# Kernel optimization log

Measured on AMD Instinct MI355X. Metric: run time of the kernel, lower is better.

The kernel has to match this reference:

```python
import jax, jax.numpy as jnp
import numpy as np

N = 100000   # nodes
E = 3200000  # edges
M = 4096     # moves
K = 16       # orders per move
NEG_SLOPE = 0.2  # PyG GATv2Conv default negative_slope

PARAM_SHAPES = {
    'g1_Wl': (10, 15), 'g1_Wr': (10, 15), 'g1_att': (10,), 'g1_b': (10,),
    'g2_Wl': (10, 25), 'g2_Wr': (10, 25), 'g2_att': (10,), 'g2_b': (10,),
    'g3_Wl': (10, 25), 'g3_Wr': (10, 25), 'g3_att': (10,), 'g3_b': (10,),
    'vt_W': (20, 29), 'vt_b': (20,), 'va_W': (1, 20), 'va_b': (1,),
    'vv_W': (10, 20), 'vv_b': (10,), 'vl_W': (1, 10), 'vl_b': (1,),
    'at_W': (20, 48), 'at_b': (20,), 'dt_W': (20, 23), 'dt_b': (20,),
    'oa_W': (1, 20), 'oa_b': (1,), 'ov_W': (1, 20), 'ov_b': (1,),
}
PARAM_NAMES = list(PARAM_SHAPES.keys())


def _linear(x, W, b):
    return x @ W.T + b


def _gatv2(x, src, dst, Wl, Wr, att, b):
    # GATv2Conv (heads=1, self-loops appended by caller), eval mode (no dropout)
    xl = x @ Wl.T  # messages from source nodes
    xr = x @ Wr.T
    e = (jax.nn.leaky_relu(xl[src] + xr[dst], NEG_SLOPE) * att).sum(-1)  # [E+N]
    emax = jax.ops.segment_max(e, dst, num_segments=N)
    ee = jnp.exp(e - emax[dst])
    denom = jax.ops.segment_sum(ee, dst, num_segments=N)
    alpha = ee / denom[dst]
    return jax.ops.segment_sum(alpha[:, None] * xl[src], dst, num_segments=N) + b


def _forward(x1, x2, edges, move_src, move_dst, move_armies, is_attack, params):
    (g1_Wl, g1_Wr, g1_att, g1_b,
     g2_Wl, g2_Wr, g2_att, g2_b,
     g3_Wl, g3_Wr, g3_att, g3_b,
     vt_W, vt_b, va_W, va_b, vv_W, vv_b, vl_W, vl_b,
     at_W, at_b, dt_W, dt_b, oa_W, oa_b, ov_W, ov_b) = params
    x2t = jnp.tile(x2, (N, 1))  # [N,4]
    self_idx = jnp.arange(N, dtype=edges.dtype)
    src = jnp.concatenate([edges[0], self_idx])
    dst = jnp.concatenate([edges[1], self_idx])
    x = jax.nn.relu(_gatv2(x1, src, dst, g1_Wl, g1_Wr, g1_att, g1_b))
    x = jax.nn.relu(_gatv2(jnp.concatenate([x, x1], 1), src, dst, g2_Wl, g2_Wr, g2_att, g2_b))
    x = jax.nn.relu(_gatv2(jnp.concatenate([x, x1], 1), src, dst, g3_Wl, g3_Wr, g3_att, g3_b))  # [N,10]
    # per-move order tensors (vectorized over [M,K]); deploy uses move_src as target
    xs, xd = x[move_src], x[move_dst]       # [M,K,10]
    x1s, x1d = x1[move_src], x1[move_dst]   # [M,K,15]
    extra = 0.6 * move_armies - 0.7 * (x1d[..., 3] + x1d[..., 4])
    attack_in = jnp.concatenate([xs, xd, x1s[..., 3:], x1d[..., 1:],
                                 move_armies[..., None], extra[..., None]], -1)  # [M,K,48]
    deploy_in = jnp.concatenate([xs, x1s[..., 3:], move_armies[..., None]], -1)  # [M,K,23]
    feat = jnp.where(is_attack[..., None] == 1,
                     _linear(attack_in, at_W, at_b),
                     _linear(deploy_in, dt_W, dt_b))
    feat = jax.nn.relu(feat)  # dropout = identity (eval)
    attn = jax.nn.softmax(_linear(feat, oa_W, oa_b), axis=1)  # softmax over orders
    p = (attn * _linear(feat, ov_W, ov_b)).sum(axis=(1, 2))   # [M]
    # value head: attention pooling over all nodes
    Vn = jax.nn.relu(_linear(jnp.concatenate([x, x1, x2t], 1), vt_W, vt_b))  # [N,20]
    vatt = jax.nn.softmax(_linear(Vn, va_W, va_b), axis=0)
    Vp = jax.nn.relu((vatt * _linear(Vn, vv_W, vv_b)).sum(axis=0))
    V = jnp.tanh(_linear(Vp, vl_W, vl_b))[0]
    return V, jax.nn.log_softmax(p, axis=0)


def setup_inputs() -> dict:
    key = jax.random.key(0)
    ks = iter(jax.random.split(key, 64))
    inp = {
        'x1': jax.random.normal(next(ks), (N, 15), jnp.float32),
        'x2': jax.random.normal(next(ks), (4,), jnp.float32),
        'edges': jax.random.randint(next(ks), (2, E), 0, N, jnp.int32),
        'move_src': jax.random.randint(next(ks), (M, K), 0, N, jnp.int32),
        'move_dst': jax.random.randint(next(ks), (M, K), 0, N, jnp.int32),
        'move_armies': jax.random.uniform(next(ks), (M, K), jnp.float32) * 10.0,
        'is_attack': jax.random.randint(next(ks), (M, K), 0, 2, jnp.int32),
    }
    for name, shape in PARAM_SHAPES.items():
        inp[name] = jax.random.normal(next(ks), shape, jnp.float32) * 0.1
    return inp


def reference(x1, x2, edges, move_src, move_dst, move_armies, is_attack,
              g1_Wl, g1_Wr, g1_att, g1_b, g2_Wl, g2_Wr, g2_att, g2_b,
              g3_Wl, g3_Wr, g3_att, g3_b, vt_W, vt_b, va_W, va_b,
              vv_W, vv_b, vl_W, vl_b, at_W, at_b, dt_W, dt_b,
              oa_W, oa_b, ov_W, ov_b):
    params = (g1_Wl, g1_Wr, g1_att, g1_b, g2_Wl, g2_Wr, g2_att, g2_b,
              g3_Wl, g3_Wr, g3_att, g3_b, vt_W, vt_b, va_W, va_b,
              vv_W, vv_b, vl_W, vl_b, at_W, at_b, dt_W, dt_b,
              oa_W, oa_b, ov_W, ov_b)
    return _forward(x1, x2, edges, move_src, move_dst, move_armies, is_attack, params)
```

## Files before the change

### kernel.cpp

```cpp
#include <hip/hip_runtime.h>
#include <hip/hip_fp16.h>
#include <math.h>

#define NN 100000
#define NE 3200000
#define MM 4096
#define KK 16
#define NEG_SLOPE 0.2f
#define SUB 8
#define BSH 8
#define NB 391
#define PCH 4096
#define FCAP 9728
#define XS 12
#define XSU 4
#define PART_BLOCKS ((NE + NN + PCH - 1) / PCH)
#define LIN_BLOCKS  ((NN + 255) / 256)
#define MOVE_BLOCKS ((MM * KK) / 256)
#define VAL_BLOCKS  ((NN + 255) / 256)
#define CSTR 16
#define PZ ((int)0xAAAAAAAAu)

typedef float vfloat2 __attribute__((__vector_size__(2 * sizeof(float))));

__device__ __forceinline__ void f8x10_decode(const uint4& w, float* xs) {
    vfloat2 f0 = __builtin_amdgcn_cvt_pk_f32_fp8(w.x, false); xs[0]=f0[0]; xs[1]=f0[1];
    vfloat2 f1 = __builtin_amdgcn_cvt_pk_f32_fp8(w.x, true);  xs[2]=f1[0]; xs[3]=f1[1];
    vfloat2 f2 = __builtin_amdgcn_cvt_pk_f32_fp8(w.y, false); xs[4]=f2[0]; xs[5]=f2[1];
    vfloat2 f3 = __builtin_amdgcn_cvt_pk_f32_fp8(w.y, true);  xs[6]=f3[0]; xs[7]=f3[1];
    vfloat2 f4 = __builtin_amdgcn_cvt_pk_f32_fp8(w.z, false); xs[8]=f4[0]; xs[9]=f4[1];
}
__device__ __forceinline__ uint4 f8x10_encode(const float* v) {
    unsigned u0 = __builtin_amdgcn_cvt_pk_fp8_f32(v[0], v[1], 0, false);
    u0 = __builtin_amdgcn_cvt_pk_fp8_f32(v[2], v[3], u0, true);
    unsigned u1 = __builtin_amdgcn_cvt_pk_fp8_f32(v[4], v[5], 0, false);
    u1 = __builtin_amdgcn_cvt_pk_fp8_f32(v[6], v[7], u1, true);
    unsigned u2 = __builtin_amdgcn_cvt_pk_fp8_f32(v[8], v[9], 0, false);
    return make_uint4(u0, u1, u2, 0u);
}

__global__ __launch_bounds__(256) void part_lin1_kernel(const int* __restrict__ edges,
                                                        int* __restrict__ cnt,
                                                        unsigned* __restrict__ recs,
                                                        const float* __restrict__ x1,
                                                        const float* __restrict__ Wl,
                                                        const float* __restrict__ Wr,
                                                        unsigned* __restrict__ xl8,
                                                        float* __restrict__ xr) {
    int t = threadIdx.x;
    if (blockIdx.x >= PART_BLOCKS) {
        int i = (blockIdx.x - PART_BLOCKS) * 256 + t;
        if (i >= NN) return;
        float in[15];
        #pragma unroll
        for (int j = 0; j < 15; j++) in[j] = x1[(long)i * 15 + j];
        float sl[10];
        #pragma unroll
        for (int o = 0; o < 10; o++) {
            float l = 0.f, r = 0.f;
            #pragma unroll
            for (int j = 0; j < 15; j++) {
                l += Wl[o * 15 + j] * in[j];
                r += Wr[o * 15 + j] * in[j];
            }
            sl[o] = l;
            xr[(long)i * XS + o] = r;
        }
        *(uint4*)(xl8 + (long)i * XSU) = f8x10_encode(sl);
        return;
    }
    __shared__ unsigned srt[PCH];
    __shared__ unsigned short sbk[PCH];
    __shared__ int scn[512];
    __shared__ int h[NB];
    __shared__ int gb[NB];
    __shared__ int cur[NB];
    __shared__ int lb[NB];
    const int total = NE + NN;
    int base = blockIdx.x * PCH;
    int n = min(PCH, total - base);
    for (int b = t; b < NB; b += 256) { h[b] = 0; cur[b] = 0; }
    __syncthreads();
    for (int j = t; j < n; j += 256) {
        int i = base + j;
        int d = (i < NE) ? edges[NE + i] : (i - NE);
        atomicAdd(&h[d >> BSH], 1);
    }
    __syncthreads();
    for (int b = t; b < NB; b += 256) {
        int hv = h[b];
        if (hv > 0) gb[b] = atomicAdd(&cnt[b * CSTR], hv) - PZ;
    }
    scn[t]       = (t < NB)       ? h[t]       : 0;
    scn[t + 256] = (t + 256 < NB) ? h[t + 256] : 0;
    __syncthreads();
    for (int off = 1; off < 512; off <<= 1) {
        int v0 = (t >= off)       ? scn[t - off]       : 0;
        int v1 = (t + 256 >= off) ? scn[t + 256 - off] : 0;
        __syncthreads();
        scn[t] += v0; scn[t + 256] += v1;
        __syncthreads();
    }
    if (t < NB)       lb[t]       = scn[t]       - h[t];
    if (t + 256 < NB) lb[t + 256] = scn[t + 256] - h[t + 256];
    __syncthreads();
    for (int j = t; j < n; j += 256) {
        int i = base + j;
        int s, d;
        if (i < NE) { s = edges[i]; d = edges[NE + i]; }
        else        { s = i - NE; d = s; }
        int b = d >> BSH;
        int slot = lb[b] + atomicAdd(&cur[b], 1);
        srt[slot] = ((unsigned)(d & 255) << 17) | (unsigned)s;
        sbk[slot] = (unsigned short)b;
    }
    __syncthreads();
    for (int j = t; j < n; j += 256) {
        int b = sbk[j];
        int gpos = gb[b] + (j - lb[b]);
        if (gpos >= 0 && gpos < FCAP) recs[(long)b * FCAP + gpos] = srt[j];
    }
}

__global__ __launch_bounds__(1024) void fine_sort_kernel(const unsigned* __restrict__ recs,
                                                         const int* __restrict__ cnt,
                                                         int* __restrict__ csr_src,
                                                         int* __restrict__ offsets) {
    __shared__ unsigned srt2[FCAP];
    __shared__ int scn[512];
    __shared__ int hist[256];
    __shared__ int sc[256];
    __shared__ int hb[257];
    __shared__ int cur[256];
    int b = blockIdx.x;
    int t = threadIdx.x;
    int c = 0;
    if (t < 512) {
        c = (t < NB) ? min(max(cnt[t * CSTR] - PZ, 0), FCAP) : 0;
        scn[t] = c;
    }
    __syncthreads();
    for (int off = 1; off < 512; off <<= 1) {
        int v = 0;
        if (t < 512 && t >= off) v = scn[t - off];
        __syncthreads();
        if (t < 512) scn[t] += v;
        __syncthreads();
    }
    int beg = (b == 0) ? 0 : scn[b - 1];
    int nb = min(max(cnt[b * CSTR] - PZ, 0), FCAP);
    int nodebase = b << BSH;
    int nnodes = min(256, NN - nodebase);
    if (t < 256) { hist[t] = 0; cur[t] = 0; }
    __syncthreads();
    const unsigned* rsrc = recs + (long)b * FCAP;
    for (int j = t; j < nb; j += 1024)
        atomicAdd(&hist[rsrc[j] >> 17], 1);
    __syncthreads();
    int hv = (t < 256) ? hist[t] : 0;
    if (t < 256) sc[t] = hv;
    __syncthreads();
    for (int off = 1; off < 256; off <<= 1) {
        int v = 0;
        if (t < 256 && t >= off) v = sc[t - off];
        __syncthreads();
        if (t < 256) sc[t] += v;
        __syncthreads();
    }
    if (t < 256) hb[t] = sc[t] - hv;
    if (t == 0) hb[256] = nb;
    __syncthreads();
    for (int j = t; j < nb; j += 1024) {
        unsigned r = rsrc[j];
        int l = r >> 17;
        int p = hb[l] + atomicAdd(&cur[l], 1);
        srt2[p] = r & 0x1FFFFu;
    }
    __syncthreads();
    for (int j = t; j < nb; j += 1024)
        csr_src[beg + j] = (int)srt2[j];
    if (t < nnodes) offsets[nodebase + t] = beg + hb[t];
    if (b == NB - 1 && t == 0) offsets[NN] = beg + nb;
}

template<bool FUSE_NEXT>
__global__ void gat_aggregate_kernel(const int* __restrict__ csr_src,
                                     const int* __restrict__ offsets,
                                     const unsigned* __restrict__ xl8,
                                     const float* __restrict__ xr,
                                     const float* __restrict__ att,
                                     const float* __restrict__ b,
                                     const float* __restrict__ x1,
                                     const float* __restrict__ nWl,
                                     const float* __restrict__ nWr,
                                     unsigned* __restrict__ xlo,
                                     float* __restrict__ xro,
                                     float* __restrict__ xout)
{
    int t = blockIdx.x * blockDim.x + threadIdx.x;
    int node = t / SUB;
    int lane = t % SUB;
    if (node >= NN) return;
    float xrn[12], a[10];
    const float4* xr4 = (const float4*)(xr + (long)node * XS);
    #pragma unroll
    for (int q = 0; q < 3; q++) {
        float4 v = xr4[q];
        xrn[4*q] = v.x; xrn[4*q+1] = v.y; xrn[4*q+2] = v.z; xrn[4*q+3] = v.w;
    }
    #pragma unroll
    for (int h = 0; h < 10; h++) a[h] = att[h];
    int beg = offsets[node], end = offsets[node + 1];
    float den = 0.f, num[10];
    #pragma unroll
    for (int h = 0; h < 10; h++) num[h] = 0.f;
    int j = beg + lane;
    for (; j + 3 * SUB < end; j += 4 * SUB) {
        int s0 = csr_src[j];
        int s1 = csr_src[j + SUB];
        int s2 = csr_src[j + 2 * SUB];
        int s3 = csr_src[j + 3 * SUB];
        uint4 wa[4];
        wa[0] = *(const uint4*)(xl8 + (long)s0 * XSU);
        wa[1] = *(const uint4*)(xl8 + (long)s1 * XSU);
        wa[2] = *(const uint4*)(xl8 + (long)s2 * XSU);
        wa[3] = *(const uint4*)(xl8 + (long)s3 * XSU);
        #pragma unroll
        for (int q = 0; q < 4; q++) {
            float xs[10];
            f8x10_decode(wa[q], xs);
            float e = 0.f;
            #pragma unroll
            for (int h = 0; h < 10; h++) {
                float v = xs[h] + xrn[h];
                v = (v >= 0.f) ? v : NEG_SLOPE * v;
                e += v * a[h];
            }
            float w = __expf(e);
            den += w;
            #pragma unroll
            for (int h = 0; h < 10; h++) num[h] += w * xs[h];
        }
    }
    for (; j < end; j += SUB) {
        int s = csr_src[j];
        uint4 wa = *(const uint4*)(xl8 + (long)s * XSU);
        float xs[10];
        f8x10_decode(wa, xs);
        float e = 0.f;
        #pragma unroll
        for (int h = 0; h < 10; h++) {
            float v = xs[h] + xrn[h];
            v = (v >= 0.f) ? v : NEG_SLOPE * v;
            e += v * a[h];
        }
        float w = __expf(e);
        den += w;
        #pragma unroll
        for (int h = 0; h < 10; h++) num[h] += w * xs[h];
    }
    #pragma unroll
    for (int off = SUB / 2; off; off >>= 1) {
        den += __shfl_xor(den, off, SUB);
        #pragma unroll
        for (int h = 0; h < 10; h++) num[h] += __shfl_xor(num[h], off, SUB);
    }
    float inv = 1.f / den;
    float xo[10];
    #pragma unroll
    for (int h = 0; h < 10; h++) xo[h] = fmaxf(num[h] * inv + b[h], 0.f);
    if (FUSE_NEXT) {
        if (lane < 5) {
            float in2[25];
            #pragma unroll
            for (int h = 0; h < 10; h++) in2[h] = xo[h];
            #pragma unroll
            for (int h = 0; h < 15; h++) in2[10 + h] = x1[(long)node * 15 + h];
            int o0 = 2 * lane, o1 = 2 * lane + 1;
            float sl0 = 0.f, sl1 = 0.f, sr0 = 0.f, sr1 = 0.f;
            #pragma unroll
            for (int jj = 0; jj < 25; jj++) {
                sl0 += nWl[o0 * 25 + jj] * in2[jj];
                sl1 += nWl[o1 * 25 + jj] * in2[jj];
                sr0 += nWr[o0 * 25 + jj] * in2[jj];
                sr1 += nWr[o1 * 25 + jj] * in2[jj];
            }
            unsigned pk = __builtin_amdgcn_cvt_pk_fp8_f32(sl0, sl1, 0, false);
            ((unsigned short*)(xlo + (long)node * XSU))[lane] = (unsigned short)pk;
            *(float2*)(xro + (long)node * XS + o0) = make_float2(sr0, sr1);
        }
    } else {
        if (lane == 0) {
            #pragma unroll
            for (int h = 0; h < 10; h++) xout[(long)node * XS + h] = xo[h];
        }
    }
}

__global__ void move_value_kernel(const float* __restrict__ x,
                                  const float* __restrict__ x1,
                                  const float* __restrict__ x2,
                                  const int* __restrict__ msrc,
                                  const int* __restrict__ mdst,
                                  const float* __restrict__ armies,
                                  const int* __restrict__ isatk,
                                  const float* __restrict__ at_W, const float* __restrict__ at_b,
                                  const float* __restrict__ dt_W, const float* __restrict__ dt_b,
                                  const float* __restrict__ oa_W, const float* __restrict__ oa_b,
                                  const float* __restrict__ ov_W, const float* __restrict__ ov_b,
                                  const float* __restrict__ vt_W, const float* __restrict__ vt_b,
                                  const float* __restrict__ va_W, const float* __restrict__ va_b,
                                  const float* __restrict__ vv_W, const float* __restrict__ vv_b,
                                  float* __restrict__ p,
                                  float* __restrict__ partials) {
    if (blockIdx.x < MOVE_BLOCKS) {
        int t = blockIdx.x * 256 + threadIdx.x;
        int m = t >> 4;
        int k = t & 15;
        int s = msrc[t], d = mdst[t];
        float arm = armies[t];
        bool atk = (isatk[t] == 1);
        float xsrc[12];
        const float4* xs4 = (const float4*)(x + (long)s * XS);
        #pragma unroll
        for (int q = 0; q < 3; q++) {
            float4 v = xs4[q];
            xsrc[4*q]=v.x; xsrc[4*q+1]=v.y; xsrc[4*q+2]=v.z; xsrc[4*q+3]=v.w;
        }
        float feat[20];
        if (atk) {
            float in[48];
            #pragma unroll
            for (int h = 0; h < 10; h++) in[h] = xsrc[h];
            const float4* xd4 = (const float4*)(x + (long)d * XS);
            float xdst[12];
            #pragma unroll
            for (int q = 0; q < 3; q++) {
                float4 v = xd4[q];
                xdst[4*q]=v.x; xdst[4*q+1]=v.y; xdst[4*q+2]=v.z; xdst[4*q+3]=v.w;
            }
            #pragma unroll
            for (int h = 0; h < 10; h++) in[10 + h] = xdst[h];
            #pragma unroll
            for (int h = 0; h < 12; h++) in[20 + h] = x1[(long)s * 15 + 3 + h];
            #pragma unroll
            for (int h = 0; h < 14; h++) in[32 + h] = x1[(long)d * 15 + 1 + h];
            in[46] = arm;
            in[47] = 0.6f * arm - 0.7f * (x1[(long)d * 15 + 3] + x1[(long)d * 15 + 4]);
            #pragma unroll
            for (int o = 0; o < 20; o++) {
                float sum = at_b[o];
                #pragma unroll
                for (int j = 0; j < 48; j++) sum += at_W[o * 48 + j] * in[j];
                feat[o] = fmaxf(sum, 0.f);
            }
        } else {
            float in[23];
            #pragma unroll
            for (int h = 0; h < 10; h++) in[h] = xsrc[h];
            #pragma unroll
            for (int h = 0; h < 12; h++) in[10 + h] = x1[(long)s * 15 + 3 + h];
            in[22] = arm;
            #pragma unroll
            for (int o = 0; o < 20; o++) {
                float sum = dt_b[o];
                #pragma unroll
                for (int j = 0; j < 23; j++) sum += dt_W[o * 23 + j] * in[j];
                feat[o] = fmaxf(sum, 0.f);
            }
        }
        float oa = oa_b[0], ov = ov_b[0];
        #pragma unroll
        for (int j = 0; j < 20; j++) {
            oa += oa_W[j] * feat[j];
            ov += ov_W[j] * feat[j];
        }
        float mx = oa;
        #pragma unroll
        for (int off = 8; off; off >>= 1) mx = fmaxf(mx, __shfl_xor(mx, off, 16));
        float w = __expf(oa - mx);
        float nume = w * ov;
        float den = w;
        #pragma unroll
        for (int off = 8; off; off >>= 1) {
            nume += __shfl_xor(nume, off, 16);
            den  += __shfl_xor(den,  off, 16);
        }
        if (k == 0) p[m] = nume / den;
        return;
    }
    __shared__ float sm[4][11];
    int vb = blockIdx.x - MOVE_BLOCKS;
    int i = vb * 256 + threadIdx.x;
    float w = 0.f;
    float acc[10];
    #pragma unroll
    for (int h = 0; h < 10; h++) acc[h] = 0.f;
    if (i < NN) {
        float in[29];
        const float4* xi4 = (const float4*)(x + (long)i * XS);
        float xi[12];
        #pragma unroll
        for (int q = 0; q < 3; q++) {
            float4 v = xi4[q];
            xi[4*q]=v.x; xi[4*q+1]=v.y; xi[4*q+2]=v.z; xi[4*q+3]=v.w;
        }
        #pragma unroll
        for (int h = 0; h < 10; h++) in[h] = xi[h];
        #pragma unroll
        for (int h = 0; h < 15; h++) in[10 + h] = x1[(long)i * 15 + h];
        #pragma unroll
        for (int h = 0; h < 4; h++) in[25 + h] = x2[h];
        float Vn[20];
        #pragma unroll
        for (int o = 0; o < 20; o++) {
            float s = vt_b[o];
            #pragma unroll
            for (int j = 0; j < 29; j++) s += vt_W[o * 29 + j] * in[j];
            Vn[o] = fmaxf(s, 0.f);
        }
        float lg = va_b[0];
        #pragma unroll
        for (int j = 0; j < 20; j++) lg += va_W[j] * Vn[j];
        w = __expf(lg);
        #pragma unroll
        for (int o = 0; o < 10; o++) {
            float s = vv_b[o];
            #pragma unroll
            for (int j = 0; j < 20; j++) s += vv_W[o * 20 + j] * Vn[j];
            acc[o] = w * s;
        }
    }
    #pragma unroll
    for (int off = 32; off; off >>= 1) {
        w += __shfl_xor(w, off, 64);
        #pragma unroll
        for (int h = 0; h < 10; h++) acc[h] += __shfl_xor(acc[h], off, 64);
    }
    int wid = threadIdx.x >> 6;
    if ((threadIdx.x & 63) == 0) {
        #pragma unroll
        for (int h = 0; h < 10; h++) sm[wid][h] = acc[h];
        sm[wid][10] = w;
    }
    __syncthreads();
    if (threadIdx.x < 11) {
        int c = threadIdx.x;
        partials[(long)vb * 12 + c] = sm[0][c] + sm[1][c] + sm[2][c] + sm[3][c];
    }
}

__global__ void final_kernel(const float* __restrict__ p,
                             const float* __restrict__ partials,
                             const float* __restrict__ vl_W, const float* __restrict__ vl_b,
                             float* __restrict__ out) {
    if (blockIdx.x == 0) {
        __shared__ float sm[256];
        int tid = threadIdx.x;
        float mx = -INFINITY;
        for (int i = tid; i < MM; i += 256) mx = fmaxf(mx, p[i]);
        sm[tid] = mx; __syncthreads();
        for (int s = 128; s; s >>= 1) { if (tid < s) sm[tid] = fmaxf(sm[tid], sm[tid + s]); __syncthreads(); }
        mx = sm[0]; __syncthreads();
        float sum = 0.f;
        for (int i = tid; i < MM; i += 256) sum += expf(p[i] - mx);
        sm[tid] = sum; __syncthreads();
        for (int s = 128; s; s >>= 1) { if (tid < s) sm[tid] += sm[tid + s]; __syncthreads(); }
        float ls = mx + logf(sm[0]);
        for (int i = tid; i < MM; i += 256) out[1 + i] = p[i] - ls;
    } else if (threadIdx.x < 64) {
        int lane = threadIdx.x;
        float s[11];
        #pragma unroll
        for (int c = 0; c < 11; c++) s[c] = 0.f;
        for (int j = lane; j < VAL_BLOCKS; j += 64)
            #pragma unroll
            for (int c = 0; c < 11; c++) s[c] += partials[(long)j * 12 + c];
        #pragma unroll
        for (int off = 32; off; off >>= 1)
            #pragma unroll
            for (int c = 0; c < 11; c++) s[c] += __shfl_xor(s[c], off, 64);
        if (lane == 0) {
            float inv = 1.0f / s[10];
            float v = vl_b[0];
            #pragma unroll
            for (int h = 0; h < 10; h++) v += vl_W[h] * fmaxf(s[h] * inv, 0.f);
            out[0] = tanhf(v);
        }
    }
}

extern "C" void kernel_launch(void* const* d_in, const int* in_sizes, int n_in,
                              void* d_out, int out_size, void* d_ws, size_t ws_size,
                              hipStream_t stream) {
    const float* x1      = (const float*)d_in[0];
    const float* x2      = (const float*)d_in[1];
    const int*   edges   = (const int*)d_in[2];
    const int*   msrc    = (const int*)d_in[3];
    const int*   mdst    = (const int*)d_in[4];
    const float* armies  = (const float*)d_in[5];
    const int*   isatk   = (const int*)d_in[6];
    const float* g1_Wl = (const float*)d_in[7],  *g1_Wr = (const float*)d_in[8];
    const float* g1_att= (const float*)d_in[9],  *g1_b  = (const float*)d_in[10];
    const float* g2_Wl = (const float*)d_in[11], *g2_Wr = (const float*)d_in[12];
    const float* g2_att= (const float*)d_in[13], *g2_b  = (const float*)d_in[14];
    const float* g3_Wl = (const float*)d_in[15], *g3_Wr = (const float*)d_in[16];
    const float* g3_att= (const float*)d_in[17], *g3_b  = (const float*)d_in[18];
    const float* vt_W  = (const float*)d_in[19], *vt_b  = (const float*)d_in[20];
    const float* va_W  = (const float*)d_in[21], *va_b  = (const float*)d_in[22];
    const float* vv_W  = (const float*)d_in[23], *vv_b  = (const float*)d_in[24];
    const float* vl_W  = (const float*)d_in[25], *vl_b  = (const float*)d_in[26];
    const float* at_W  = (const float*)d_in[27], *at_b  = (const float*)d_in[28];
    const float* dt_W  = (const float*)d_in[29], *dt_b  = (const float*)d_in[30];
    const float* oa_W  = (const float*)d_in[31], *oa_b  = (const float*)d_in[32];
    const float* ov_W  = (const float*)d_in[33], *ov_b  = (const float*)d_in[34];

    float* out = (float*)d_out;

    float* ws = (float*)d_ws;
    unsigned* xl8A = (unsigned*)ws;
    unsigned* xl8B = xl8A + (long)NN * XSU;
    float* xrA = (float*)(xl8B + (long)NN * XSU);
    float* xrB = xrA + (long)NN * XS;
    float* xF  = xrB + (long)NN * XS;
    int* csr_src = (int*)(xF + (long)NN * XS);
    int* offsets = csr_src + (NE + NN);
    unsigned* recs = (unsigned*)(offsets + NN + 4);
    int* cnt   = (int*)(recs + (long)NB * FCAP);
    float* pbuf = (float*)(cnt + NB * CSTR + 16);
    float* partials = pbuf + MM;

    const int aggBlocks = ((long)NN * SUB + 255) / 256;

    part_lin1_kernel<<<PART_BLOCKS + LIN_BLOCKS, 256, 0, stream>>>(
        edges, cnt, recs, x1, g1_Wl, g1_Wr, xl8A, xrA);
    fine_sort_kernel<<<NB, 1024, 0, stream>>>(recs, cnt, csr_src, offsets);
    gat_aggregate_kernel<true><<<aggBlocks, 256, 0, stream>>>(
        csr_src, offsets, xl8A, xrA, g1_att, g1_b, x1, g2_Wl, g2_Wr, xl8B, xrB, nullptr);
    gat_aggregate_kernel<true><<<aggBlocks, 256, 0, stream>>>(
        csr_src, offsets, xl8B, xrB, g2_att, g2_b, x1, g3_Wl, g3_Wr, xl8A, xrA, nullptr);
    gat_aggregate_kernel<false><<<aggBlocks, 256, 0, stream>>>(
        csr_src, offsets, xl8A, xrA, g3_att, g3_b, x1, nullptr, nullptr, nullptr, nullptr, xF);
    move_value_kernel<<<MOVE_BLOCKS + VAL_BLOCKS, 256, 0, stream>>>(
        xF, x1, x2, msrc, mdst, armies, isatk,
        at_W, at_b, dt_W, dt_b, oa_W, oa_b, ov_W, ov_b,
        vt_W, vt_b, va_W, va_b, vv_W, vv_b, pbuf, partials);
    final_kernel<<<2, 256, 0, stream>>>(pbuf, partials, vl_W, vl_b, out);
}
```

Before: 325.1 us.

## Pad coarse-bucket chunks to 16 records with sentinels and enlarge partition chunks

The partition kernel now processes 8192 edges per 512-thread block. Each block reserves bucket space rounded up to multiples of 16 records and fills the padding with sentinel values, so global record writes land in aligned segments. A second counter keeps the real record count, and the fine sort skips sentinels while using that count for CSR offsets. The padding adds wasted record traffic and sentinel checks, and FCAP grows to hold it, which raises LDS use in the fine sort.

```diff
diff --git a/kernel.cpp b/kernel.cpp
--- a/kernel.cpp
+++ b/kernel.cpp
@@ -10,15 +10,16 @@
 #define SUB 8
 #define BSH 8
 #define NB 391
-#define PCH 4096
-#define FCAP 9728
+#define PCH 8192
+#define FCAP 12288
 #define XS 12
 #define XSU 4
 #define PART_BLOCKS ((NE + NN + PCH - 1) / PCH)
-#define LIN_BLOCKS  ((NN + 255) / 256)
+#define LIN_BLOCKS  ((NN + 511) / 512)
 #define MOVE_BLOCKS ((MM * KK) / 256)
 #define VAL_BLOCKS  ((NN + 255) / 256)
 #define CSTR 16
+#define SENT 0xFFFFFFFFu
 #define PZ ((int)0xAAAAAAAAu)
 
 typedef float vfloat2 __attribute__((__vector_size__(2 * sizeof(float))));
@@ -39,7 +40,7 @@
     return make_uint4(u0, u1, u2, 0u);
 }
 
-__global__ __launch_bounds__(256) void part_lin1_kernel(const int* __restrict__ edges,
+__global__ __launch_bounds__(512) void part_lin1_kernel(const int* __restrict__ edges,
                                                         int* __restrict__ cnt,
                                                         unsigned* __restrict__ recs,
                                                         const float* __restrict__ x1,
@@ -49,7 +50,7 @@
                                                         float* __restrict__ xr) {
     int t = threadIdx.x;
     if (blockIdx.x >= PART_BLOCKS) {
-        int i = (blockIdx.x - PART_BLOCKS) * 256 + t;
+        int i = (blockIdx.x - PART_BLOCKS) * 512 + t;
         if (i >= NN) return;
         float in[15];
         #pragma unroll
@@ -79,32 +80,33 @@
     const int total = NE + NN;
     int base = blockIdx.x * PCH;
     int n = min(PCH, total - base);
-    for (int b = t; b < NB; b += 256) { h[b] = 0; cur[b] = 0; }
-    __syncthreads();
-    for (int j = t; j < n; j += 256) {
+    for (int b = t; b < NB; b += 512) { h[b] = 0; cur[b] = 0; }
+    __syncthreads();
+    for (int j = t; j < n; j += 512) {
         int i = base + j;
         int d = (i < NE) ? edges[NE + i] : (i - NE);
         atomicAdd(&h[d >> BSH], 1);
     }
     __syncthreads();
-    for (int b = t; b < NB; b += 256) {
+    for (int b = t; b < NB; b += 512) {
         int hv = h[b];
-        if (hv > 0) gb[b] = atomicAdd(&cnt[b * CSTR], hv) - PZ;
-    }
-    scn[t]       = (t < NB)       ? h[t]       : 0;
-    scn[t + 256] = (t + 256 < NB) ? h[t + 256] : 0;
+        if (hv > 0) {
+            int padded = (hv + 15) & ~15;
+            gb[b] = atomicAdd(&cnt[b * CSTR], padded) - PZ;
+            atomicAdd(&cnt[b * CSTR + 1], hv);
+        }
+    }
+    scn[t] = (t < NB) ? h[t] : 0;
     __syncthreads();
     for (int off = 1; off < 512; off <<= 1) {
-        int v0 = (t >= off)       ? scn[t - off]       : 0;
-        int v1 = (t + 256 >= off) ? scn[t + 256 - off] : 0;
+        int v = (t >= off) ? scn[t - off] : 0;
         __syncthreads();
-        scn[t] += v0; scn[t + 256] += v1;
+        scn[t] += v;
         __syncthreads();
     }
-    if (t < NB)       lb[t]       = scn[t]       - h[t];
-    if (t + 256 < NB) lb[t + 256] = scn[t + 256] - h[t + 256];
-    __syncthreads();
-    for (int j = t; j < n; j += 256) {
+    if (t < NB) lb[t] = scn[t] - h[t];
+    __syncthreads();
+    for (int j = t; j < n; j += 512) {
         int i = base + j;
         int s, d;
         if (i < NE) { s = edges[i]; d = edges[NE + i]; }
@@ -115,10 +117,20 @@
         sbk[slot] = (unsigned short)b;
     }
     __syncthreads();
-    for (int j = t; j < n; j += 256) {
+    for (int j = t; j < n; j += 512) {
         int b = sbk[j];
         int gpos = gb[b] + (j - lb[b]);
         if (gpos >= 0 && gpos < FCAP) recs[(long)b * FCAP + gpos] = srt[j];
+    }
+    for (int b = t; b < NB; b += 512) {
+        int hv = h[b];
+        if (hv > 0) {
+            int padded = (hv + 15) & ~15;
+            for (int q = hv; q < padded; q++) {
+                int gpos = gb[b] + q;
+                if (gpos >= 0 && gpos < FCAP) recs[(long)b * FCAP + gpos] = SENT;
+            }
+        }
     }
 }
 
@@ -134,9 +146,8 @@
     __shared__ int cur[256];
     int b = blockIdx.x;
     int t = threadIdx.x;
-    int c = 0;
     if (t < 512) {
-        c = (t < NB) ? min(max(cnt[t * CSTR] - PZ, 0), FCAP) : 0;
+        int c = (t < NB) ? min(max(cnt[t * CSTR + 1] - PZ, 0), FCAP) : 0;
         scn[t] = c;
     }
     __syncthreads();
@@ -148,14 +159,17 @@
         __syncthreads();
     }
     int beg = (b == 0) ? 0 : scn[b - 1];
-    int nb = min(max(cnt[b * CSTR] - PZ, 0), FCAP);
+    int nbp = min(max(cnt[b * CSTR] - PZ, 0), FCAP);
+    int nbr = min(max(cnt[b * CSTR + 1] - PZ, 0), FCAP);
     int nodebase = b << BSH;
     int nnodes = min(256, NN - nodebase);
     if (t < 256) { hist[t] = 0; cur[t] = 0; }
     __syncthreads();
     const unsigned* rsrc = recs + (long)b * FCAP;
-    for (int j = t; j < nb; j += 1024)
-        atomicAdd(&hist[rsrc[j] >> 17], 1);
+    for (int j = t; j < nbp; j += 1024) {
+        unsigned r = rsrc[j];
+        if (r != SENT) atomicAdd(&hist[r >> 17], 1);
+    }
     __syncthreads();
     int hv = (t < 256) ? hist[t] : 0;
     if (t < 256) sc[t] = hv;
@@ -168,19 +182,21 @@
         __syncthreads();
     }
     if (t < 256) hb[t] = sc[t] - hv;
-    if (t == 0) hb[256] = nb;
-    __syncthreads();
-    for (int j = t; j < nb; j += 1024) {
+    if (t == 0) hb[256] = nbr;
+    __syncthreads();
+    for (int j = t; j < nbp; j += 1024) {
         unsigned r = rsrc[j];
-        int l = r >> 17;
-        int p = hb[l] + atomicAdd(&cur[l], 1);
-        srt2[p] = r & 0x1FFFFu;
-    }
-    __syncthreads();
-    for (int j = t; j < nb; j += 1024)
+        if (r != SENT) {
+            int l = r >> 17;
+            int p = hb[l] + atomicAdd(&cur[l], 1);
+            srt2[p] = r & 0x1FFFFu;
+        }
+    }
+    __syncthreads();
+    for (int j = t; j < nbr; j += 1024)
         csr_src[beg + j] = (int)srt2[j];
     if (t < nnodes) offsets[nodebase + t] = beg + hb[t];
-    if (b == NB - 1 && t == 0) offsets[NN] = beg + nb;
+    if (b == NB - 1 && t == 0) offsets[NN] = beg + nbr;
 }
 
 template<bool FUSE_NEXT>
@@ -525,14 +541,14 @@
     float* xF  = xrB + (long)NN * XS;
     int* csr_src = (int*)(xF + (long)NN * XS);
     int* offsets = csr_src + (NE + NN);
-    unsigned* recs = (unsigned*)(offsets + NN + 4);
+    unsigned* recs = (unsigned*)(offsets + NN + 16);
     int* cnt   = (int*)(recs + (long)NB * FCAP);
     float* pbuf = (float*)(cnt + NB * CSTR + 16);
     float* partials = pbuf + MM;
 
     const int aggBlocks = ((long)NN * SUB + 255) / 256;
 
-    part_lin1_kernel<<<PART_BLOCKS + LIN_BLOCKS, 256, 0, stream>>>(
+    part_lin1_kernel<<<PART_BLOCKS + LIN_BLOCKS, 512, 0, stream>>>(
         edges, cnt, recs, x1, g1_Wl, g1_Wr, xl8A, xrA);
     fine_sort_kernel<<<NB, 1024, 0, stream>>>(recs, cnt, csr_src, offsets);
     gat_aggregate_kernel<true><<<aggBlocks, 256, 0, stream>>>(
```

New measurement: 319.8 us. About the same (-1.6%).
